# Optimization experiments

Measured on AMD Instinct MI355X. Metric: run time of the kernel, lower is better.

The kernel has to match this reference:

```python
import jax, jax.numpy as jnp
import numpy as np

B, LR_DIM, G_DIM, K, D, T = 256, 1024, 512, 64, 256, 8
GRID = jnp.linspace(-4.0, 4.0, 41)  # registered buffer in torch module


def _mu_bell(x, c, a_bell, b_bell):
    # generalized bell membership, clamp(a,b) >= 1e-3 as in torch
    a = jnp.maximum(a_bell, 1e-3)
    b = jnp.maximum(b_bell, 1e-3)
    return 1.0 / (1.0 + jnp.abs((x - c) / a) ** (2.0 * b))


def _mu_s(x, a, b):
    eps = 1e-12
    a2 = jnp.minimum(a, b)
    b2 = jnp.maximum(a, b)
    mid = (a2 + b2) * 0.5
    up = 2.0 * ((x - a2) / (b2 - a2 + eps)) ** 2
    dn = 1.0 - 2.0 * ((b2 - x) / (b2 - a2 + eps)) ** 2
    y = jnp.where((x > a2) & (x <= mid), up, jnp.zeros_like(x))
    y = jnp.where((x > mid) & (x <= b2), dn, y)
    return jnp.where(x > b2, jnp.ones_like(x), y)


def _fuzzify(x, a_bell, b_bell):
    # x: (B,d) -> (B,2d)
    xs = 4.0 * jnp.tanh(x / 4.0)
    xb = _mu_bell(xs, 0.0, a_bell, b_bell)
    xS = _mu_s(xs, -1.0, 1.0)
    return jnp.concatenate([xb, xS], axis=-1)


def _defuzzify(rt, a_bell, b_bell):
    # rt: (B,2d) -> centroid (B,d)
    d = rt.shape[1] // 2
    rb, rs = rt[:, :d], rt[:, d:]
    g = GRID[None, None, :]                      # (1,1,G)
    c_b = 4.0 * jnp.tanh(rb)[..., None]          # (B,d,1)
    c_s = 4.0 * jnp.tanh(rs)[..., None]
    mu_b = _mu_bell(g, c_b, a_bell, b_bell)      # (B,d,G)
    a_s = jnp.clip(c_s - 1.0, -4.0, 4.0)
    b_s = jnp.clip(c_s + 1.0, -4.0, 4.0)
    mu_s = _mu_s(g, a_s, b_s)
    cen_b = (g * mu_b).sum(-1) / (mu_b.sum(-1) + 1e-12)
    cen_s = (g * mu_s).sum(-1) / (mu_s.sum(-1) + 1e-12)
    return 0.5 * cen_b + 0.5 * cen_s


def _forward(wsi_lr, genomics, FT, W_lr, b_lr, W_g, b_g, WqI, WqG, WkI, WkG,
             WvI, WvG, mlp_W1, mlp_b1, mlp_W2, mlp_b2, Wf, bf, Wi, bi, Vf, Vi,
             a_bell, b_bell):
    scale = jnp.float32(D) ** 0.5
    lr = wsi_lr @ W_lr + b_lr                    # (B,d)
    g = genomics @ W_g + b_g
    lr_f = _fuzzify(lr, a_bell, b_bell)          # (B,2d)
    g_f = _fuzzify(g, a_bell, b_bell)
    QI = lr_f @ WqI                              # (B,d), loop-invariant
    QG = g_f @ WqG
    Ft0 = jnp.broadcast_to(FT[None], (wsi_lr.shape[0],) + FT.shape)  # (B,K,d)

    def step(Ft, _):
        sI = jnp.einsum('bd,bkd->bk', QI, Ft @ WkI) / scale
        sG = jnp.einsum('bd,bkd->bk', QG, Ft @ WkG) / scale
        rtI = jnp.einsum('bk,bke->be', jax.nn.softmax(sI, axis=-1), Ft @ WvI)  # (B,2d)
        rtG = jnp.einsum('bk,bke->be', jax.nn.softmax(sG, axis=-1), Ft @ WvG)
        r = 0.5 * _defuzzify(rtI, a_bell, b_bell) + 0.5 * _defuzzify(rtG, a_bell, b_bell)
        rb = jnp.broadcast_to(r[:, None, :], Ft.shape)              # (B,K,d)
        x = Ft + rb
        F_tilde = jax.nn.gelu(x @ mlp_W1 + mlp_b1, approximate=False) @ mlp_W2 + mlp_b2 + x
        f_gate = jax.nn.sigmoid(rb @ Wf + bf + jnp.tanh(Ft @ Vf))
        i_gate = jax.nn.sigmoid(rb @ Wi + bi + jnp.tanh(Ft @ Vi))
        Ft_new = f_gate * Ft + i_gate * jnp.tanh(F_tilde)
        return Ft_new, Ft_new

    _, steps = jax.lax.scan(step, Ft0, None, length=T)
    # torch stores step `T-s` result at index s-1: list index 0 holds the LAST
    # computed state, index T-1 the first -> reverse chronological order
    return steps[::-1]  # (T,B,K,d)


def setup_inputs() -> dict:
    key = jax.random.key(0)
    ks = jax.random.split(key, 20)

    def rn(k, shape, scale):
        return jax.random.normal(k, shape, dtype=jnp.float32) * scale

    z = lambda *s: jnp.zeros(s, jnp.float32)
    return dict(
        wsi_lr=rn(ks[0], (B, LR_DIM), 1.0),
        genomics=rn(ks[1], (B, G_DIM), 1.0),
        FT=rn(ks[2], (K, D), 0.02),
        W_lr=rn(ks[3], (LR_DIM, D), LR_DIM ** -0.5), b_lr=z(D),
        W_g=rn(ks[4], (G_DIM, D), G_DIM ** -0.5), b_g=z(D),
        WqI=rn(ks[5], (2 * D, D), (2 * D) ** -0.5),
        WqG=rn(ks[6], (2 * D, D), (2 * D) ** -0.5),
        WkI=rn(ks[7], (D, D), D ** -0.5),
        WkG=rn(ks[8], (D, D), D ** -0.5),
        WvI=rn(ks[9], (D, 2 * D), D ** -0.5),
        WvG=rn(ks[10], (D, 2 * D), D ** -0.5),
        mlp_W1=rn(ks[11], (D, 2 * D), D ** -0.5), mlp_b1=z(2 * D),
        mlp_W2=rn(ks[12], (2 * D, D), (2 * D) ** -0.5), mlp_b2=z(D),
        Wf=rn(ks[13], (D, D), D ** -0.5), bf=z(D),
        Wi=rn(ks[14], (D, D), D ** -0.5), bi=z(D),
        Vf=rn(ks[15], (D, D), D ** -0.5),
        Vi=rn(ks[16], (D, D), D ** -0.5),
        a_bell=jnp.float32(1.0),
        b_bell=jnp.float32(2.0),
    )


def reference(wsi_lr, genomics, FT, W_lr, b_lr, W_g, b_g, WqI, WqG, WkI, WkG,
              WvI, WvG, mlp_W1, mlp_b1, mlp_W2, mlp_b2, Wf, bf, Wi, bi, Vf, Vi,
              a_bell, b_bell):
    return _forward(wsi_lr, genomics, FT, W_lr, b_lr, W_g, b_g, WqI, WqG, WkI,
                    WkG, WvI, WvG, mlp_W1, mlp_b1, mlp_W2, mlp_b2, Wf, bf, Wi,
                    bi, Vf, Vi, a_bell, b_bell)
```

## Files before the change

kernel.cpp:

```cpp
#include <hip/hip_runtime.h>
#include <hip/hip_bf16.h>

#define B_    256
#define K_    64
#define D_    256
#define T_    8
#define NROW  (B_*K_)

typedef short short8v __attribute__((ext_vector_type(8)));
typedef float f32x4  __attribute__((ext_vector_type(4)));

__device__ __forceinline__ float fexp2(float x) { return __builtin_amdgcn_exp2f(x); }
__device__ __forceinline__ float flog2(float x) { return __builtin_amdgcn_logf(x); }

__device__ __forceinline__ float sigmoid_f(float x) {
  return 1.f / (1.f + fexp2(x * -1.4426950408889634f));
}
__device__ __forceinline__ float tanh_fast(float x) {
  float xc = fminf(fmaxf(x, -30.f), 30.f);
  float t = fexp2(xc * 2.8853900817779268f);
  return (t - 1.f) / (t + 1.f);
}
__device__ __forceinline__ float gelu_f(float x) {
  return 0.5f * x * (1.f + erff(x * 0.70710678118654752440f));
}
__device__ __forceinline__ unsigned short f2bf(float x) {
  __hip_bfloat16 h = __float2bfloat16(x);
  return *reinterpret_cast<unsigned short*>(&h);
}
__device__ __forceinline__ float bfss(unsigned short s) {
  return __uint_as_float(((unsigned int)s) << 16);
}
__device__ __forceinline__ float muS_f(float x, float a2, float b2) {
  float mid = 0.5f * (a2 + b2);
  float inv = 1.f / (b2 - a2 + 1e-12f);
  if (x > b2)  return 1.f;
  if (x > mid) { float u = (b2 - x) * inv; return 1.f - 2.f * u * u; }
  if (x > a2)  { float u = (x - a2) * inv; return 2.f * u * u; }
  return 0.f;
}
__device__ __forceinline__ float pow_abs(float z, float e2b) {
  return fexp2(e2b * flog2(fabsf(z)));
}
__device__ __forceinline__ float defuzz_one(float rb_, float rs_, float ab, float bb) {
  float e2b = 2.f * bb;
  float inv_ab = 1.f / ab;
  float cb = 4.f * tanh_fast(rb_);
  float num = 0.f, den = 0.f;
  #pragma unroll
  for (int j = 0; j < 41; ++j) {
    float gj = -4.f + 0.2f * (float)j;
    float mu = 1.f / (1.f + pow_abs((gj - cb) * inv_ab, e2b));
    num += gj * mu; den += mu;
  }
  float cenb = num / (den + 1e-12f);
  float cs = 4.f * tanh_fast(rs_);
  float as_ = fminf(fmaxf(cs - 1.f, -4.f), 4.f);
  float bs_ = fminf(fmaxf(cs + 1.f, -4.f), 4.f);
  num = 0.f; den = 0.f;
  {
    float mid = 0.5f * (as_ + bs_);
    float inv = 1.f / (bs_ - as_ + 1e-12f);
    #pragma unroll
    for (int j = 0; j < 41; ++j) {
      float gj = -4.f + 0.2f * (float)j;
      float mu;
      if (gj > bs_)      mu = 1.f;
      else if (gj > mid) { float u = (bs_ - gj) * inv; mu = 1.f - 2.f * u * u; }
      else if (gj > as_) { float u = (gj - as_) * inv; mu = 2.f * u * u; }
      else               mu = 0.f;
      num += gj * mu; den += mu;
    }
  }
  float cens = num / (den + 1e-12f);
  return 0.5f * cenb + 0.5f * cens;
}

__global__ __launch_bounds__(256) void k_convert(
    const float* __restrict__ W1, const float* __restrict__ Vf, const float* __restrict__ Vi,
    const float* __restrict__ W2, const float* __restrict__ FT,
    const float* __restrict__ WkI, const float* __restrict__ WkG,
    const float* __restrict__ WvI, const float* __restrict__ WvG,
    const float* __restrict__ Wf,  const float* __restrict__ Wi,
    unsigned short* __restrict__ B1t, unsigned short* __restrict__ W2t,
    unsigned short* __restrict__ FTbf,
    float* __restrict__ WkIt, float* __restrict__ WkGt,
    unsigned short* __restrict__ Wv2, unsigned short* __restrict__ WB)
{
  int idx = blockIdx.x * 256 + threadIdx.x;
  if (idx < 262144) {
    int n = idx >> 8, k = idx & 255;
    float v = (n < 512) ? W1[(size_t)k*512 + n]
            : (n < 768) ? Vf[(size_t)k*256 + (n-512)]
                        : Vi[(size_t)k*256 + (n-768)];
    B1t[idx] = f2bf(v);
  } else if (idx < 393216) {
    int j = idx - 262144;
    int n = j >> 9, k = j & 511;
    W2t[j] = f2bf(W2[(size_t)k*256 + n]);
  } else if (idx < 409600) {
    int j = idx - 393216;
    FTbf[j] = f2bf(FT[j]);
  } else if (idx < 475136) {
    int j = idx - 409600;
    int k = j >> 8, n = j & 255;
    WkIt[j] = WkI[(size_t)n*256 + k];
  } else if (idx < 540672) {
    int j = idx - 475136;
    int k = j >> 8, n = j & 255;
    WkGt[j] = WkG[(size_t)n*256 + k];
  } else if (idx < 802816) {
    int j = idx - 540672;
    int d = j >> 10, c = j & 1023;
    float v = (c < 512) ? WvI[(size_t)d*512 + c] : WvG[(size_t)d*512 + (c-512)];
    Wv2[j] = f2bf(v);
  } else if (idx < 1064960) {
    int j = idx - 802816;
    int d = j >> 10, c = j & 1023;
    float v = (c < 512) ? W1[(size_t)d*512 + c]
            : (c < 768) ? Wf[(size_t)d*256 + (c-512)]
                        : Wi[(size_t)d*256 + (c-768)];
    WB[j] = f2bf(v);
  }
}

__global__ __launch_bounds__(256) void k_pre_lin(
    const float* __restrict__ wsi, const float* __restrict__ gen,
    const float* __restrict__ W_lr, const float* __restrict__ b_lr,
    const float* __restrict__ W_g,  const float* __restrict__ b_g,
    const float* __restrict__ a_p,  const float* __restrict__ b_p,
    float* __restrict__ lrf, float* __restrict__ gf)
{
  int g_ix = blockIdx.x;
  int half = g_ix >> 4, tile = g_ix & 15;
  int bx = tile & 3, by = tile >> 2;
  int n0 = bx * 64, m0 = by * 64;
  const float* A    = half ? gen  : wsi;
  const float* Bm   = half ? W_g  : W_lr;
  const float* bias = half ? b_g  : b_lr;
  float* outp       = half ? gf   : lrf;
  int KK            = half ? 512  : 1024;
  float ab = fmaxf(a_p[0], 0.001f), bb = fmaxf(b_p[0], 0.001f);
  float e2b = 2.f * bb, inv_ab = 1.f / ab;

  __shared__ float As[16][64];
  __shared__ float Bs[16][64];
  int tid = threadIdx.x, tx = tid & 15, ty = tid >> 4;
  float acc[4][4] = {};
  int am = tid >> 2, ak = (tid & 3) * 4;
  int bk = tid >> 4, bn = (tid & 15) * 4;
  const float* arow = A + (size_t)(m0 + am) * KK;
  for (int k0 = 0; k0 < KK; k0 += 16) {
    float4 av = *(const float4*)(arow + k0 + ak);
    As[ak+0][am] = av.x; As[ak+1][am] = av.y; As[ak+2][am] = av.z; As[ak+3][am] = av.w;
    *(float4*)&Bs[bk][bn] = *(const float4*)(Bm + (size_t)(k0 + bk) * 256 + n0 + bn);
    __syncthreads();
    #pragma unroll
    for (int kk = 0; kk < 16; ++kk) {
      float a0 = As[kk][ty*4+0], a1 = As[kk][ty*4+1], a2 = As[kk][ty*4+2], a3 = As[kk][ty*4+3];
      float b0 = Bs[kk][tx*4+0], b1 = Bs[kk][tx*4+1], b2 = Bs[kk][tx*4+2], b3 = Bs[kk][tx*4+3];
      acc[0][0]=fmaf(a0,b0,acc[0][0]); acc[0][1]=fmaf(a0,b1,acc[0][1]); acc[0][2]=fmaf(a0,b2,acc[0][2]); acc[0][3]=fmaf(a0,b3,acc[0][3]);
      acc[1][0]=fmaf(a1,b0,acc[1][0]); acc[1][1]=fmaf(a1,b1,acc[1][1]); acc[1][2]=fmaf(a1,b2,acc[1][2]); acc[1][3]=fmaf(a1,b3,acc[1][3]);
      acc[2][0]=fmaf(a2,b0,acc[2][0]); acc[2][1]=fmaf(a2,b1,acc[2][1]); acc[2][2]=fmaf(a2,b2,acc[2][2]); acc[2][3]=fmaf(a2,b3,acc[2][3]);
      acc[3][0]=fmaf(a3,b0,acc[3][0]); acc[3][1]=fmaf(a3,b1,acc[3][1]); acc[3][2]=fmaf(a3,b2,acc[3][2]); acc[3][3]=fmaf(a3,b3,acc[3][3]);
    }
    __syncthreads();
  }
  #pragma unroll
  for (int i = 0; i < 4; ++i) {
    int row = m0 + ty*4 + i;
    #pragma unroll
    for (int j = 0; j < 4; ++j) {
      int col = n0 + tx*4 + j;
      float v = acc[i][j] + bias[col];
      float xs = 4.f * tanh_fast(v * 0.25f);
      outp[(size_t)row*512 + col]       = 1.f / (1.f + pow_abs(xs * inv_ab, e2b));
      outp[(size_t)row*512 + col + 256] = muS_f(xs, -1.f, 1.f);
    }
  }
}

__global__ __launch_bounds__(256) void k_pre_q(
    const float* __restrict__ lrf, const float* __restrict__ gf,
    const float* __restrict__ WqI, const float* __restrict__ WqG,
    float* __restrict__ QI, float* __restrict__ QG)
{
  int g_ix = blockIdx.x;
  int half = g_ix >> 4, tile = g_ix & 15;
  int bx = tile & 3, by = tile >> 2;
  int n0 = bx * 64, m0 = by * 64;
  const float* A  = half ? gf  : lrf;
  const float* Bm = half ? WqG : WqI;
  float* outp     = half ? QG  : QI;

  __shared__ float As[16][64];
  __shared__ float Bs[16][64];
  int tid = threadIdx.x, tx = tid & 15, ty = tid >> 4;
  float acc[4][4] = {};
  int am = tid >> 2, ak = (tid & 3) * 4;
  int bk = tid >> 4, bn = (tid & 15) * 4;
  const float* arow = A + (size_t)(m0 + am) * 512;
  for (int k0 = 0; k0 < 512; k0 += 16) {
    float4 av = *(const float4*)(arow + k0 + ak);
    As[ak+0][am] = av.x; As[ak+1][am] = av.y; As[ak+2][am] = av.z; As[ak+3][am] = av.w;
    *(float4*)&Bs[bk][bn] = *(const float4*)(Bm + (size_t)(k0 + bk) * 256 + n0 + bn);
    __syncthreads();
    #pragma unroll
    for (int kk = 0; kk < 16; ++kk) {
      float a0 = As[kk][ty*4+0], a1 = As[kk][ty*4+1], a2 = As[kk][ty*4+2], a3 = As[kk][ty*4+3];
      float b0 = Bs[kk][tx*4+0], b1 = Bs[kk][tx*4+1], b2 = Bs[kk][tx*4+2], b3 = Bs[kk][tx*4+3];
      acc[0][0]=fmaf(a0,b0,acc[0][0]); acc[0][1]=fmaf(a0,b1,acc[0][1]); acc[0][2]=fmaf(a0,b2,acc[0][2]); acc[0][3]=fmaf(a0,b3,acc[0][3]);
      acc[1][0]=fmaf(a1,b0,acc[1][0]); acc[1][1]=fmaf(a1,b1,acc[1][1]); acc[1][2]=fmaf(a1,b2,acc[1][2]); acc[1][3]=fmaf(a1,b3,acc[1][3]);
      acc[2][0]=fmaf(a2,b0,acc[2][0]); acc[2][1]=fmaf(a2,b1,acc[2][1]); acc[2][2]=fmaf(a2,b2,acc[2][2]); acc[2][3]=fmaf(a2,b3,acc[2][3]);
      acc[3][0]=fmaf(a3,b0,acc[3][0]); acc[3][1]=fmaf(a3,b1,acc[3][1]); acc[3][2]=fmaf(a3,b2,acc[3][2]); acc[3][3]=fmaf(a3,b3,acc[3][3]);
    }
    __syncthreads();
  }
  #pragma unroll
  for (int i = 0; i < 4; ++i) {
    float4 v = make_float4(acc[i][0], acc[i][1], acc[i][2], acc[i][3]);
    *(float4*)(outp + (size_t)(m0 + ty*4 + i) * 256 + n0 + tx*4) = v;
  }
}

__global__ __launch_bounds__(256) void k_pre_qp(
    const float* __restrict__ QI, const float* __restrict__ QG,
    const float* __restrict__ WkIt, const float* __restrict__ WkGt,
    float* __restrict__ qIp, float* __restrict__ qGp)
{
  int g_ix = blockIdx.x;
  int half = g_ix >> 4, tile = g_ix & 15;
  int bx = tile & 3, by = tile >> 2;
  int n0 = bx * 64, m0 = by * 64;
  const float* A  = half ? QG   : QI;
  const float* Bm = half ? WkGt : WkIt;
  float* outp     = half ? qGp  : qIp;

  __shared__ float As[16][64];
  __shared__ float Bs[16][64];
  int tid = threadIdx.x, tx = tid & 15, ty = tid >> 4;
  float acc[4][4] = {};
  int am = tid >> 2, ak = (tid & 3) * 4;
  int bk = tid >> 4, bn = (tid & 15) * 4;
  const float* arow = A + (size_t)(m0 + am) * 256;
  for (int k0 = 0; k0 < 256; k0 += 16) {
    float4 av = *(const float4*)(arow + k0 + ak);
    As[ak+0][am] = av.x; As[ak+1][am] = av.y; As[ak+2][am] = av.z; As[ak+3][am] = av.w;
    *(float4*)&Bs[bk][bn] = *(const float4*)(Bm + (size_t)(k0 + bk) * 256 + n0 + bn);
    __syncthreads();
    #pragma unroll
    for (int kk = 0; kk < 16; ++kk) {
      float a0 = As[kk][ty*4+0], a1 = As[kk][ty*4+1], a2 = As[kk][ty*4+2], a3 = As[kk][ty*4+3];
      float b0 = Bs[kk][tx*4+0], b1 = Bs[kk][tx*4+1], b2 = Bs[kk][tx*4+2], b3 = Bs[kk][tx*4+3];
      acc[0][0]=fmaf(a0,b0,acc[0][0]); acc[0][1]=fmaf(a0,b1,acc[0][1]); acc[0][2]=fmaf(a0,b2,acc[0][2]); acc[0][3]=fmaf(a0,b3,acc[0][3]);
      acc[1][0]=fmaf(a1,b0,acc[1][0]); acc[1][1]=fmaf(a1,b1,acc[1][1]); acc[1][2]=fmaf(a1,b2,acc[1][2]); acc[1][3]=fmaf(a1,b3,acc[1][3]);
      acc[2][0]=fmaf(a2,b0,acc[2][0]); acc[2][1]=fmaf(a2,b1,acc[2][1]); acc[2][2]=fmaf(a2,b2,acc[2][2]); acc[2][3]=fmaf(a2,b3,acc[2][3]);
      acc[3][0]=fmaf(a3,b0,acc[3][0]); acc[3][1]=fmaf(a3,b1,acc[3][1]); acc[3][2]=fmaf(a3,b2,acc[3][2]); acc[3][3]=fmaf(a3,b3,acc[3][3]);
    }
    __syncthreads();
  }
  #pragma unroll
  for (int i = 0; i < 4; ++i) {
    float4 v = make_float4(acc[i][0], acc[i][1], acc[i][2], acc[i][3]);
    *(float4*)(outp + (size_t)(m0 + ty*4 + i) * 256 + n0 + tx*4) = v;
  }
}

__global__ __launch_bounds__(256, 2) void k_step1(
    const unsigned short* __restrict__ Fb_all, int bcast,
    const unsigned short* __restrict__ B1t,
    const float* __restrict__ qIp, const float* __restrict__ qGp,
    const unsigned short* __restrict__ Wv2, const unsigned short* __restrict__ WB,
    const float* __restrict__ a_p, const float* __restrict__ b_p,
    unsigned short* __restrict__ U1, unsigned short* __restrict__ Tf, unsigned short* __restrict__ Ti,
    float* __restrict__ rr, float* __restrict__ rW1,
    float* __restrict__ rWf, float* __restrict__ rWi)
{
  __shared__ __align__(16) char smem[38912];
  int bid = blockIdx.x, tid = threadIdx.x;

  if (bid >= 256) {
    int gb = bid - 256;
    int bx = gb & 7, by = gb >> 3;
    int n0 = bx * 128, m0 = by * 128;
    short* As = (short*)smem;
    short* Bs = As + 128*72;
    int w = tid >> 6, wm = w >> 1, wn = w & 1, lane = tid & 63, lr = lane & 15, lh = lane >> 4;
    f32x4 acc[4][4] = {};
    int srow = tid >> 3, koff = (tid & 7) * 8;
    for (int k0 = 0; k0 < 256; k0 += 64) {
      #pragma unroll
      for (int rnd = 0; rnd < 4; ++rnd) {
        int rrow = rnd * 32 + srow;
        int ar = bcast ? ((m0 + rrow) & 63) : (m0 + rrow);
        *(float4*)&As[rrow*72 + koff] = *(const float4*)&Fb_all[(size_t)ar * 256 + k0 + koff];
        *(float4*)&Bs[rrow*72 + koff] = *(const float4*)&B1t[(size_t)(n0 + rrow) * 256 + k0 + koff];
      }
      __syncthreads();
      #pragma unroll
      for (int ks = 0; ks < 2; ++ks) {
        short8v a[4], b[4];
        #pragma unroll
        for (int m = 0; m < 4; ++m) a[m] = *(const short8v*)&As[(wm*64 + m*16 + lr)*72 + ks*32 + lh*8];
        #pragma unroll
        for (int n = 0; n < 4; ++n) b[n] = *(const short8v*)&Bs[(wn*64 + n*16 + lr)*72 + ks*32 + lh*8];
        #pragma unroll
        for (int m = 0; m < 4; ++m)
          #pragma unroll
          for (int n = 0; n < 4; ++n)
            acc[m][n] = __builtin_amdgcn_mfma_f32_16x16x32_bf16(a[m], b[n], acc[m][n], 0, 0, 0);
      }
      __syncthreads();
    }
    if (bx < 4) {
      #pragma unroll
      for (int n = 0; n < 4; ++n) {
        int col = n0 + wn*64 + n*16 + lr;
        #pragma unroll
        for (int m = 0; m < 4; ++m) {
          int rbase = m0 + wm*64 + m*16 + lh*4;
          #pragma unroll
          for (int r = 0; r < 4; ++r)
            U1[(size_t)(rbase + r) * 512 + col] = f2bf(acc[m][n][r]);
        }
      }
    } else {
      int isI = (bx >= 6);
      unsigned short* outp = isI ? Ti : Tf;
      int cb = isI ? 768 : 512;
      #pragma unroll
      for (int n = 0; n < 4; ++n) {
        int c = n0 + wn*64 + n*16 + lr - cb;
        #pragma unroll
        for (int m = 0; m < 4; ++m) {
          int rbase = m0 + wm*64 + m*16 + lh*4;
          #pragma unroll
          for (int r = 0; r < 4; ++r)
            outp[(size_t)(rbase + r) * 256 + c] = f2bf(tanh_fast(acc[m][n][r]));
        }
      }
    }
    return;
  }

  int b = bid, t = tid;
  short* Fs  = (short*)smem;
  float* qv  = (float*)(smem + 33792);
  float* red = (float*)(smem + 35840);
  float* prl = (float*)(smem + 37888);
  float* ftb = red;

  const unsigned short* Fsrc = bcast ? Fb_all : (Fb_all + (size_t)b * K_ * D_);
  #pragma unroll
  for (int i = 0; i < 8; ++i) {
    int sidx = (i * 256 + t) * 8;
    int row = sidx >> 8, col = sidx & 255;
    *(float4*)&Fs[row * 264 + col] = *(const float4*)&Fsrc[sidx];
  }
  qv[t]       = qIp[(size_t)b*256 + t];
  qv[256 + t] = qGp[(size_t)b*256 + t];
  __syncthreads();

  {
    int k = t & 63, part = t >> 6;
    const unsigned int* frow = (const unsigned int*)&Fs[k * 264 + part * 64];
    const float* q0 = qv + part * 64;
    const float* q1 = qv + 256 + part * 64;
    float s0 = 0.f, s1 = 0.f;
    #pragma unroll
    for (int d2 = 0; d2 < 32; ++d2) {
      unsigned int pr = frow[d2];
      float f0 = __uint_as_float(pr << 16);
      float f1 = __uint_as_float(pr & 0xffff0000u);
      s0 = fmaf(f1, q0[2*d2+1], fmaf(f0, q0[2*d2], s0));
      s1 = fmaf(f1, q1[2*d2+1], fmaf(f0, q1[2*d2], s1));
    }
    red[t] = s0; red[256 + t] = s1;
  }
  __syncthreads();
  if (t < 128) {
    int which = t >> 6, kk = t & 63;
    const float* rp = red + which * 256;
    float s = (rp[kk] + rp[64+kk] + rp[128+kk] + rp[192+kk]) * (1.f/16.f);
    float m = s;
    for (int off = 32; off; off >>= 1) m = fmaxf(m, __shfl_xor(m, off, 64));
    float e = fexp2((s - m) * 1.4426950408889634f);
    float sum = e;
    for (int off = 32; off; off >>= 1) sum += __shfl_xor(sum, off, 64);
    prl[which * 64 + kk] = e / sum;
  }
  __syncthreads();
  {
    float f0 = 0.f, f1 = 0.f;
    #pragma unroll 8
    for (int kk = 0; kk < 64; ++kk) {
      float fv = bfss((unsigned short)Fs[kk * 264 + t]);
      f0 = fmaf(prl[kk],      fv, f0);
      f1 = fmaf(prl[64 + kk], fv, f1);
    }
    __syncthreads();
    ftb[t] = f0; ftb[256 + t] = f1;
  }
  __syncthreads();
  float aI0 = 0.f, aI1 = 0.f, aG0 = 0.f, aG1 = 0.f;
  #pragma unroll 4
  for (int d = 0; d < 256; ++d) {
    float fI = ftb[d], fG = ftb[256 + d];
    const unsigned short* wr = Wv2 + ((size_t)d << 10);
    aI0 = fmaf(fI, bfss(wr[t]),       aI0);
    aI1 = fmaf(fI, bfss(wr[t + 256]), aI1);
    aG0 = fmaf(fG, bfss(wr[512 + t]), aG0);
    aG1 = fmaf(fG, bfss(wr[768 + t]), aG1);
  }
  {
    float ab = fmaxf(a_p[0], 0.001f), bb = fmaxf(b_p[0], 0.001f);
    float rI = defuzz_one(aI0, aI1, ab, bb);
    float rG = defuzz_one(aG0, aG1, ab, bb);
    float rv = 0.5f * rI + 0.5f * rG;
    __syncthreads();
    prl[t] = rv;
    rr[(size_t)b*256 + t] = rv;
  }
  __syncthreads();
  {
    float w0 = 0.f, w1 = 0.f, wf = 0.f, wi = 0.f;
    #pragma unroll 4
    for (int d = 0; d < 256; ++d) {
      float rv = prl[d];
      const unsigned short* wr = WB + ((size_t)d << 10);
      w0 = fmaf(rv, bfss(wr[t]),       w0);
      w1 = fmaf(rv, bfss(wr[t + 256]), w1);
      wf = fmaf(rv, bfss(wr[512 + t]), wf);
      wi = fmaf(rv, bfss(wr[768 + t]), wi);
    }
    rW1[(size_t)b*512 + t]       = w0;
    rW1[(size_t)b*512 + t + 256] = w1;
    rWf[(size_t)b*256 + t] = wf;
    rWi[(size_t)b*256 + t] = wi;
  }
}

__global__ __launch_bounds__(256) void mfma_gemm2(
    const unsigned short* __restrict__ U1, const unsigned short* __restrict__ W2t,
    const float* __restrict__ b1, const float* __restrict__ b2,
    const float* __restrict__ rW1,
    const float* __restrict__ Fprev, const float* __restrict__ FT, int bcast,
    const float* __restrict__ rr,
    const float* __restrict__ rWf, const float* __restrict__ bfv,
    const float* __restrict__ rWi, const float* __restrict__ biv,
    const unsigned short* __restrict__ Tf, const unsigned short* __restrict__ Ti,
    float* __restrict__ Fout, unsigned short* __restrict__ Fbf)
{
  int bx = blockIdx.x & 1, by = blockIdx.x >> 1;
  int n0 = bx * 128, m0 = by * 64;
  __shared__ __align__(16) short As[64][72];
  __shared__ __align__(16) short Bs[128][72];
  int tid = threadIdx.x;
  int w = tid >> 6, lane = tid & 63, lr = lane & 15, lh = lane >> 4;
  f32x4 acc[4][2] = {};
  int srow = tid >> 3, koff = (tid & 7) * 8;
  const float* rwrow = rW1 + (size_t)by * 512;

  for (int k0 = 0; k0 < 512; k0 += 64) {
    float add_[8];
    #pragma unroll
    for (int q = 0; q < 8; ++q) add_[q] = rwrow[k0 + koff + q] + b1[k0 + koff + q];
    #pragma unroll
    for (int rnd = 0; rnd < 2; ++rnd) {
      int rrow = rnd * 32 + srow;
      int row = m0 + rrow;
      uint4 u = *(const uint4*)&U1[(size_t)row * 512 + k0 + koff];
      unsigned int uu[4] = {u.x, u.y, u.z, u.w};
      unsigned int pk[4];
      #pragma unroll
      for (int q = 0; q < 4; ++q) {
        float lo = __uint_as_float(uu[q] << 16)         + add_[2*q];
        float hi = __uint_as_float(uu[q] & 0xffff0000u) + add_[2*q+1];
        pk[q] = (((unsigned int)f2bf(gelu_f(hi))) << 16) | f2bf(gelu_f(lo));
      }
      uint4 pv; pv.x = pk[0]; pv.y = pk[1]; pv.z = pk[2]; pv.w = pk[3];
      *(uint4*)&As[rrow][koff] = pv;
    }
    #pragma unroll
    for (int rnd = 0; rnd < 4; ++rnd) {
      int rrow = rnd * 32 + srow;
      *(float4*)&Bs[rrow][koff] = *(const float4*)&W2t[(size_t)(n0 + rrow) * 512 + k0 + koff];
    }
    __syncthreads();
    #pragma unroll
    for (int ks = 0; ks < 2; ++ks) {
      short8v a[4], b[2];
      #pragma unroll
      for (int m = 0; m < 4; ++m) a[m] = *(const short8v*)&As[m*16 + lr][ks*32 + lh*8];
      #pragma unroll
      for (int n = 0; n < 2; ++n) b[n] = *(const short8v*)&Bs[w*32 + n*16 + lr][ks*32 + lh*8];
      #pragma unroll
      for (int m = 0; m < 4; ++m)
        #pragma unroll
        for (int n = 0; n < 2; ++n)
          acc[m][n] = __builtin_amdgcn_mfma_f32_16x16x32_bf16(a[m], b[n], acc[m][n], 0, 0, 0);
    }
    __syncthreads();
  }

  int bnum = by;
  const float* rp = rr + (size_t)bnum * 256;
  #pragma unroll
  for (int n = 0; n < 2; ++n) {
    int col = n0 + w*32 + n*16 + lr;
    float b2c = b2[col], rv = rp[col];
    float gf_ = rWf[(size_t)bnum*256 + col] + bfv[col];
    float gi_ = rWi[(size_t)bnum*256 + col] + biv[col];
    #pragma unroll
    for (int m = 0; m < 4; ++m) {
      int rbase = m0 + m*16 + lh*4;
      #pragma unroll
      for (int r = 0; r < 4; ++r) {
        int row = rbase + r;
        float Ftv = bcast ? FT[(size_t)(row & 63) * 256 + col]
                          : Fprev[(size_t)row * 256 + col];
        float ftld = acc[m][n][r] + b2c + Ftv + rv;
        float fg = sigmoid_f(gf_ + bfss(Tf[(size_t)row * 256 + col]));
        float ig = sigmoid_f(gi_ + bfss(Ti[(size_t)row * 256 + col]));
        float ov = fg * Ftv + ig * tanh_fast(ftld);
        Fout[(size_t)row * 256 + col] = ov;
        Fbf[(size_t)row * 256 + col] = f2bf(ov);
      }
    }
  }
}

extern "C" void kernel_launch(void* const* d_in, const int* in_sizes, int n_in,
                              void* d_out, int out_size, void* d_ws, size_t ws_size,
                              hipStream_t stream)
{
  (void)in_sizes; (void)n_in; (void)out_size; (void)ws_size;
  const float* wsi  = (const float*)d_in[0];
  const float* gen  = (const float*)d_in[1];
  const float* FT   = (const float*)d_in[2];
  const float* W_lr = (const float*)d_in[3];
  const float* b_lr = (const float*)d_in[4];
  const float* W_g  = (const float*)d_in[5];
  const float* b_g  = (const float*)d_in[6];
  const float* WqI  = (const float*)d_in[7];
  const float* WqG  = (const float*)d_in[8];
  const float* WkI  = (const float*)d_in[9];
  const float* WkG  = (const float*)d_in[10];
  const float* WvI  = (const float*)d_in[11];
  const float* WvG  = (const float*)d_in[12];
  const float* W1   = (const float*)d_in[13];
  const float* b1   = (const float*)d_in[14];
  const float* W2   = (const float*)d_in[15];
  const float* b2   = (const float*)d_in[16];
  const float* Wf   = (const float*)d_in[17];
  const float* bf   = (const float*)d_in[18];
  const float* Wi   = (const float*)d_in[19];
  const float* bi   = (const float*)d_in[20];
  const float* Vf   = (const float*)d_in[21];
  const float* Vi   = (const float*)d_in[22];
  const float* a_p  = (const float*)d_in[23];
  const float* b_p  = (const float*)d_in[24];

  float* out = (float*)d_out;
  float* ws  = (float*)d_ws;
  float* rr    = ws;
  float* rW1   = rr    + 65536;
  float* rWf   = rW1   + 131072;
  float* rWi   = rWf   + 65536;
  float* qIp   = rWi   + 65536;
  float* qGp   = qIp   + 65536;
  float* lrf   = qGp   + 65536;
  float* gf    = lrf   + 131072;
  float* QI    = gf    + 131072;
  float* QG    = QI    + 65536;
  float* WkIt  = QG    + 65536;
  float* WkGt  = WkIt  + 65536;
  unsigned short* U1   = (unsigned short*)(WkGt + 65536);
  unsigned short* Tfb  = U1   + 8388608;
  unsigned short* Tib  = Tfb  + 4194304;
  unsigned short* Fbf  = Tib  + 4194304;
  unsigned short* FTbf = Fbf  + 4194304;
  unsigned short* B1t  = FTbf + 16384;
  unsigned short* W2t  = B1t  + 262144;
  unsigned short* Wv2  = W2t  + 131072;
  unsigned short* WB   = Wv2  + 262144;

  k_convert<<<4160, 256, 0, stream>>>(W1, Vf, Vi, W2, FT, WkI, WkG, WvI, WvG, Wf, Wi,
                                      B1t, W2t, FTbf, WkIt, WkGt, Wv2, WB);
  k_pre_lin<<<32, 256, 0, stream>>>(wsi, gen, W_lr, b_lr, W_g, b_g, a_p, b_p, lrf, gf);
  k_pre_q<<<32, 256, 0, stream>>>(lrf, gf, WqI, WqG, QI, QG);
  k_pre_qp<<<32, 256, 0, stream>>>(QI, QG, WkIt, WkGt, qIp, qGp);

  const float* Fcur = nullptr;
  int bcast = 1;
  for (int st = 0; st < T_; ++st) {
    float* Fnext = out + (size_t)(7 - st) * NROW * D_;
    k_step1<<<1280, 256, 0, stream>>>(bcast ? FTbf : Fbf, bcast, B1t, qIp, qGp,
                                      Wv2, WB, a_p, b_p,
                                      U1, Tfb, Tib, rr, rW1, rWf, rWi);
    mfma_gemm2<<<512, 256, 0, stream>>>(U1, W2t, b1, b2, rW1, Fcur, FT, bcast, rr,
                                        rWf, bf, rWi, bi, Tfb, Tib, Fnext, Fbf);
    Fcur = Fnext;
    bcast = 0;
  }
}
```

Measured before the change: 1.077 ms.

## Split per-batch matvec tail of step kernel into tiled fp32 GEMM kernels

The per-batch vector-matrix products (attention value projection, defuzzify, and the r·[W1|Wf|Wi] projections) move out of the fused step kernel into separate tiled fp32 GEMM kernels over all batches. Before, each batch block streamed the full bf16 weight matrices by itself, and those blocks sat alongside the MFMA GEMM blocks in one launch. The new kernels share weight tiles across 64 rows and read the original fp32 weights, so the bf16 conversions of WvI/WvG/W1/Wf/Wi are dropped and the launch bound relaxes. In exchange there are three more launches per step and intermediate round trips through global memory, and the tail kernels launch only 64 blocks each, which is low occupancy.

```diff
diff --git a/kernel.cpp b/kernel.cpp
--- a/kernel.cpp
+++ b/kernel.cpp
@@ -80,12 +80,9 @@
     const float* __restrict__ W1, const float* __restrict__ Vf, const float* __restrict__ Vi,
     const float* __restrict__ W2, const float* __restrict__ FT,
     const float* __restrict__ WkI, const float* __restrict__ WkG,
-    const float* __restrict__ WvI, const float* __restrict__ WvG,
-    const float* __restrict__ Wf,  const float* __restrict__ Wi,
     unsigned short* __restrict__ B1t, unsigned short* __restrict__ W2t,
     unsigned short* __restrict__ FTbf,
-    float* __restrict__ WkIt, float* __restrict__ WkGt,
-    unsigned short* __restrict__ Wv2, unsigned short* __restrict__ WB)
+    float* __restrict__ WkIt, float* __restrict__ WkGt)
 {
   int idx = blockIdx.x * 256 + threadIdx.x;
   if (idx < 262144) {
@@ -109,18 +106,6 @@
     int j = idx - 475136;
     int k = j >> 8, n = j & 255;
     WkGt[j] = WkG[(size_t)n*256 + k];
-  } else if (idx < 802816) {
-    int j = idx - 540672;
-    int d = j >> 10, c = j & 1023;
-    float v = (c < 512) ? WvI[(size_t)d*512 + c] : WvG[(size_t)d*512 + (c-512)];
-    Wv2[j] = f2bf(v);
-  } else if (idx < 1064960) {
-    int j = idx - 802816;
-    int d = j >> 10, c = j & 1023;
-    float v = (c < 512) ? W1[(size_t)d*512 + c]
-            : (c < 768) ? Wf[(size_t)d*256 + (c-512)]
-                        : Wi[(size_t)d*256 + (c-768)];
-    WB[j] = f2bf(v);
   }
 }
 
@@ -266,22 +251,18 @@
   }
 }
 
-__global__ __launch_bounds__(256, 2) void k_step1(
+__global__ __launch_bounds__(256) void k_stepA(
     const unsigned short* __restrict__ Fb_all, int bcast,
     const unsigned short* __restrict__ B1t,
     const float* __restrict__ qIp, const float* __restrict__ qGp,
-    const unsigned short* __restrict__ Wv2, const unsigned short* __restrict__ WB,
-    const float* __restrict__ a_p, const float* __restrict__ b_p,
     unsigned short* __restrict__ U1, unsigned short* __restrict__ Tf, unsigned short* __restrict__ Ti,
-    float* __restrict__ rr, float* __restrict__ rW1,
-    float* __restrict__ rWf, float* __restrict__ rWi)
+    float* __restrict__ ftbI, float* __restrict__ ftbG)
 {
   __shared__ __align__(16) char smem[38912];
   int bid = blockIdx.x, tid = threadIdx.x;
 
-  if (bid >= 256) {
-    int gb = bid - 256;
-    int bx = gb & 7, by = gb >> 3;
+  if (bid < 1024) {
+    int bx = bid & 7, by = bid >> 3;
     int n0 = bx * 128, m0 = by * 128;
     short* As = (short*)smem;
     short* Bs = As + 128*72;
@@ -343,12 +324,11 @@
     return;
   }
 
-  int b = bid, t = tid;
+  int b = bid - 1024, t = tid;
   short* Fs  = (short*)smem;
   float* qv  = (float*)(smem + 33792);
   float* red = (float*)(smem + 35840);
   float* prl = (float*)(smem + 37888);
-  float* ftb = red;
 
   const unsigned short* Fsrc = bcast ? Fb_all : (Fb_all + (size_t)b * K_ * D_);
   #pragma unroll
@@ -360,7 +340,6 @@
   qv[t]       = qIp[(size_t)b*256 + t];
   qv[256 + t] = qGp[(size_t)b*256 + t];
   __syncthreads();
-
   {
     int k = t & 63, part = t >> 6;
     const unsigned int* frow = (const unsigned int*)&Fs[k * 264 + part * 64];
@@ -398,45 +377,106 @@
       f0 = fmaf(prl[kk],      fv, f0);
       f1 = fmaf(prl[64 + kk], fv, f1);
     }
-    __syncthreads();
-    ftb[t] = f0; ftb[256 + t] = f1;
-  }
-  __syncthreads();
-  float aI0 = 0.f, aI1 = 0.f, aG0 = 0.f, aG1 = 0.f;
-  #pragma unroll 4
-  for (int d = 0; d < 256; ++d) {
-    float fI = ftb[d], fG = ftb[256 + d];
-    const unsigned short* wr = Wv2 + ((size_t)d << 10);
-    aI0 = fmaf(fI, bfss(wr[t]),       aI0);
-    aI1 = fmaf(fI, bfss(wr[t + 256]), aI1);
-    aG0 = fmaf(fG, bfss(wr[512 + t]), aG0);
-    aG1 = fmaf(fG, bfss(wr[768 + t]), aG1);
-  }
-  {
-    float ab = fmaxf(a_p[0], 0.001f), bb = fmaxf(b_p[0], 0.001f);
-    float rI = defuzz_one(aI0, aI1, ab, bb);
-    float rG = defuzz_one(aG0, aG1, ab, bb);
-    float rv = 0.5f * rI + 0.5f * rG;
-    __syncthreads();
-    prl[t] = rv;
-    rr[(size_t)b*256 + t] = rv;
-  }
-  __syncthreads();
-  {
-    float w0 = 0.f, w1 = 0.f, wf = 0.f, wi = 0.f;
-    #pragma unroll 4
-    for (int d = 0; d < 256; ++d) {
-      float rv = prl[d];
-      const unsigned short* wr = WB + ((size_t)d << 10);
-      w0 = fmaf(rv, bfss(wr[t]),       w0);
-      w1 = fmaf(rv, bfss(wr[t + 256]), w1);
-      wf = fmaf(rv, bfss(wr[512 + t]), wf);
-      wi = fmaf(rv, bfss(wr[768 + t]), wi);
-    }
-    rW1[(size_t)b*512 + t]       = w0;
-    rW1[(size_t)b*512 + t + 256] = w1;
-    rWf[(size_t)b*256 + t] = wf;
-    rWi[(size_t)b*256 + t] = wi;
+    ftbI[(size_t)b*256 + t] = f0;
+    ftbG[(size_t)b*256 + t] = f1;
+  }
+}
+
+__global__ __launch_bounds__(256) void k_rt(
+    const float* __restrict__ ftbI, const float* __restrict__ ftbG,
+    const float* __restrict__ WvI,  const float* __restrict__ WvG,
+    float* __restrict__ rt)
+{
+  int bx = blockIdx.x & 15, by = blockIdx.x >> 4;
+  int n0 = bx * 64, m0 = by * 64;
+  const float* Ap = (n0 < 512) ? ftbI : ftbG;
+  const float* Bp = (n0 < 512) ? WvI  : WvG;
+  int nb = (n0 < 512) ? n0 : n0 - 512;
+  __shared__ float As[16][64];
+  __shared__ float Bs[16][64];
+  int tid = threadIdx.x, tx = tid & 15, ty = tid >> 4;
+  float acc[4][4] = {};
+  int am = tid >> 2, ak = (tid & 3) * 4;
+  int bk = tid >> 4, bn = (tid & 15) * 4;
+  const float* arow = Ap + (size_t)(m0 + am) * 256;
+  for (int k0 = 0; k0 < 256; k0 += 16) {
+    float4 av = *(const float4*)(arow + k0 + ak);
+    As[ak+0][am] = av.x; As[ak+1][am] = av.y; As[ak+2][am] = av.z; As[ak+3][am] = av.w;
+    *(float4*)&Bs[bk][bn] = *(const float4*)(Bp + (size_t)(k0 + bk) * 512 + nb + bn);
+    __syncthreads();
+    #pragma unroll
+    for (int kk = 0; kk < 16; ++kk) {
+      float a0 = As[kk][ty*4+0], a1 = As[kk][ty*4+1], a2 = As[kk][ty*4+2], a3 = As[kk][ty*4+3];
+      float b0 = Bs[kk][tx*4+0], b1 = Bs[kk][tx*4+1], b2 = Bs[kk][tx*4+2], b3 = Bs[kk][tx*4+3];
+      acc[0][0]=fmaf(a0,b0,acc[0][0]); acc[0][1]=fmaf(a0,b1,acc[0][1]); acc[0][2]=fmaf(a0,b2,acc[0][2]); acc[0][3]=fmaf(a0,b3,acc[0][3]);
+      acc[1][0]=fmaf(a1,b0,acc[1][0]); acc[1][1]=fmaf(a1,b1,acc[1][1]); acc[1][2]=fmaf(a1,b2,acc[1][2]); acc[1][3]=fmaf(a1,b3,acc[1][3]);
+      acc[2][0]=fmaf(a2,b0,acc[2][0]); acc[2][1]=fmaf(a2,b1,acc[2][1]); acc[2][2]=fmaf(a2,b2,acc[2][2]); acc[2][3]=fmaf(a2,b3,acc[2][3]);
+      acc[3][0]=fmaf(a3,b0,acc[3][0]); acc[3][1]=fmaf(a3,b1,acc[3][1]); acc[3][2]=fmaf(a3,b2,acc[3][2]); acc[3][3]=fmaf(a3,b3,acc[3][3]);
+    }
+    __syncthreads();
+  }
+  #pragma unroll
+  for (int i = 0; i < 4; ++i) {
+    float4 v = make_float4(acc[i][0], acc[i][1], acc[i][2], acc[i][3]);
+    *(float4*)(rt + (size_t)(m0 + ty*4 + i) * 1024 + n0 + tx*4) = v;
+  }
+}
+
+__global__ __launch_bounds__(256) void k_defuzz(
+    const float* __restrict__ rt,
+    const float* __restrict__ a_p, const float* __restrict__ b_p,
+    float* __restrict__ r_out)
+{
+  int b = blockIdx.x, t = threadIdx.x;
+  float ab = fmaxf(a_p[0], 0.001f), bb = fmaxf(b_p[0], 0.001f);
+  const float* rb = rt + (size_t)b * 1024;
+  float rI = defuzz_one(rb[t],       rb[256 + t], ab, bb);
+  float rG = defuzz_one(rb[512 + t], rb[768 + t], ab, bb);
+  r_out[(size_t)b*256 + t] = 0.5f * rI + 0.5f * rG;
+}
+
+__global__ __launch_bounds__(256) void k_rW(
+    const float* __restrict__ r,
+    const float* __restrict__ W1, const float* __restrict__ Wf, const float* __restrict__ Wi,
+    float* __restrict__ rW1, float* __restrict__ rWf, float* __restrict__ rWi)
+{
+  int bx = blockIdx.x & 15, by = blockIdx.x >> 4;
+  int n0 = bx * 64, m0 = by * 64;
+  const float* Bp; int ldb, nb;
+  if (n0 < 512)      { Bp = W1; ldb = 512; nb = n0; }
+  else if (n0 < 768) { Bp = Wf; ldb = 256; nb = n0 - 512; }
+  else               { Bp = Wi; ldb = 256; nb = n0 - 768; }
+  __shared__ float As[16][64];
+  __shared__ float Bs[16][64];
+  int tid = threadIdx.x, tx = tid & 15, ty = tid >> 4;
+  float acc[4][4] = {};
+  int am = tid >> 2, ak = (tid & 3) * 4;
+  int bk = tid >> 4, bn = (tid & 15) * 4;
+  const float* arow = r + (size_t)(m0 + am) * 256;
+  for (int k0 = 0; k0 < 256; k0 += 16) {
+    float4 av = *(const float4*)(arow + k0 + ak);
+    As[ak+0][am] = av.x; As[ak+1][am] = av.y; As[ak+2][am] = av.z; As[ak+3][am] = av.w;
+    *(float4*)&Bs[bk][bn] = *(const float4*)(Bp + (size_t)(k0 + bk) * ldb + nb + bn);
+    __syncthreads();
+    #pragma unroll
+    for (int kk = 0; kk < 16; ++kk) {
+      float a0 = As[kk][ty*4+0], a1 = As[kk][ty*4+1], a2 = As[kk][ty*4+2], a3 = As[kk][ty*4+3];
+      float b0 = Bs[kk][tx*4+0], b1 = Bs[kk][tx*4+1], b2 = Bs[kk][tx*4+2], b3 = Bs[kk][tx*4+3];
+      acc[0][0]=fmaf(a0,b0,acc[0][0]); acc[0][1]=fmaf(a0,b1,acc[0][1]); acc[0][2]=fmaf(a0,b2,acc[0][2]); acc[0][3]=fmaf(a0,b3,acc[0][3]);
+      acc[1][0]=fmaf(a1,b0,acc[1][0]); acc[1][1]=fmaf(a1,b1,acc[1][1]); acc[1][2]=fmaf(a1,b2,acc[1][2]); acc[1][3]=fmaf(a1,b3,acc[1][3]);
+      acc[2][0]=fmaf(a2,b0,acc[2][0]); acc[2][1]=fmaf(a2,b1,acc[2][1]); acc[2][2]=fmaf(a2,b2,acc[2][2]); acc[2][3]=fmaf(a2,b3,acc[2][3]);
+      acc[3][0]=fmaf(a3,b0,acc[3][0]); acc[3][1]=fmaf(a3,b1,acc[3][1]); acc[3][2]=fmaf(a3,b2,acc[3][2]); acc[3][3]=fmaf(a3,b3,acc[3][3]);
+    }
+    __syncthreads();
+  }
+  #pragma unroll
+  for (int i = 0; i < 4; ++i) {
+    int row = m0 + ty*4 + i;
+    float4 v = make_float4(acc[i][0], acc[i][1], acc[i][2], acc[i][3]);
+    int c = tx * 4;
+    if (n0 < 512)      *(float4*)(rW1 + (size_t)row*512 + n0 + c)        = v;
+    else if (n0 < 768) *(float4*)(rWf + (size_t)row*256 + (n0-512) + c)  = v;
+    else               *(float4*)(rWi + (size_t)row*256 + (n0-768) + c)  = v;
   }
 }
 
@@ -575,18 +615,19 @@
   float* QG    = QI    + 65536;
   float* WkIt  = QG    + 65536;
   float* WkGt  = WkIt  + 65536;
-  unsigned short* U1   = (unsigned short*)(WkGt + 65536);
+  float* ftbI  = WkGt  + 65536;
+  float* ftbG  = ftbI  + 65536;
+  float* rt    = ftbG  + 65536;
+  unsigned short* U1   = (unsigned short*)(rt + 262144);
   unsigned short* Tfb  = U1   + 8388608;
   unsigned short* Tib  = Tfb  + 4194304;
   unsigned short* Fbf  = Tib  + 4194304;
   unsigned short* FTbf = Fbf  + 4194304;
   unsigned short* B1t  = FTbf + 16384;
   unsigned short* W2t  = B1t  + 262144;
-  unsigned short* Wv2  = W2t  + 131072;
-  unsigned short* WB   = Wv2  + 262144;
-
-  k_convert<<<4160, 256, 0, stream>>>(W1, Vf, Vi, W2, FT, WkI, WkG, WvI, WvG, Wf, Wi,
-                                      B1t, W2t, FTbf, WkIt, WkGt, Wv2, WB);
+
+  k_convert<<<2112, 256, 0, stream>>>(W1, Vf, Vi, W2, FT, WkI, WkG,
+                                      B1t, W2t, FTbf, WkIt, WkGt);
   k_pre_lin<<<32, 256, 0, stream>>>(wsi, gen, W_lr, b_lr, W_g, b_g, a_p, b_p, lrf, gf);
   k_pre_q<<<32, 256, 0, stream>>>(lrf, gf, WqI, WqG, QI, QG);
   k_pre_qp<<<32, 256, 0, stream>>>(QI, QG, WkIt, WkGt, qIp, qGp);
@@ -595,9 +636,11 @@
   int bcast = 1;
   for (int st = 0; st < T_; ++st) {
     float* Fnext = out + (size_t)(7 - st) * NROW * D_;
-    k_step1<<<1280, 256, 0, stream>>>(bcast ? FTbf : Fbf, bcast, B1t, qIp, qGp,
-                                      Wv2, WB, a_p, b_p,
-                                      U1, Tfb, Tib, rr, rW1, rWf, rWi);
+    k_stepA<<<1280, 256, 0, stream>>>(bcast ? FTbf : Fbf, bcast, B1t, qIp, qGp,
+                                      U1, Tfb, Tib, ftbI, ftbG);
+    k_rt<<<64, 256, 0, stream>>>(ftbI, ftbG, WvI, WvG, rt);
+    k_defuzz<<<256, 256, 0, stream>>>(rt, a_p, b_p, rr);
+    k_rW<<<64, 256, 0, stream>>>(rr, W1, Wf, Wi, rW1, rWf, rWi);
     mfma_gemm2<<<512, 256, 0, stream>>>(U1, W2t, b1, b2, rW1, Fcur, FT, bcast, rr,
                                         rWf, bf, rWi, bi, Tfb, Tib, Fnext, Fbf);
     Fcur = Fnext;
```

New measurement: 1.100 ms. 2.2% more time.
